# Performance work log

Hardware: AMD Instinct MI355X
Metric: run time of the kernel (lower is better)

## Reference

```python
import jax, jax.numpy as jnp
import numpy as np

EPS = 1e-5
BOUNDARY = 1.0 - EPS
TEMP = 0.5  # temperature from init_kwargs


def _safe_sqrt(t):
    # sqrt with zero (not inf/nan) gradient at t<=0; matches the analytic clamp
    # in the original custom backward (clamp(z*beta, min=eps)).
    pos = t > 0
    return jnp.where(pos, jnp.sqrt(jnp.where(pos, t, 1.0)), 0.0)


def _poincare_sim(z):
    # z: [2N, D]. Pairwise Poincare distance computed via the matmul identity
    # ||u-v||^2 = ||u||^2 + ||v||^2 - 2 u.v instead of a (2N,2N,D) broadcast.
    raw = jnp.sum(z * z, axis=-1)                      # [2N] unclamped sq norms
    sqc = jnp.clip(raw, 0.0, BOUNDARY)                 # clamped as in forward
    sqdist = jnp.maximum(raw[:, None] + raw[None, :] - 2.0 * (z @ z.T), 0.0)
    x = sqdist / ((1.0 - sqc[:, None]) * (1.0 - sqc[None, :])) * 2.0 + 1.0
    dist = jnp.log(x + _safe_sqrt(x * x - 1.0))        # arcosh(x)
    return 1.0 / (1.0 + dist)                          # Poincare similarity


def setup_inputs() -> dict:
    key = jax.random.key(0)
    k1, k2, k3, k4 = jax.random.split(key, 4)
    N, D = 4096, 8

    def ball(kg, kr):
        g = jax.random.normal(kg, (N, D), dtype=jnp.float32)
        r = jax.random.uniform(kr, (N, 1), dtype=jnp.float32) * 0.85
        return g * r / (jnp.linalg.norm(g, axis=-1, keepdims=True) + 1e-6)

    return {"z_i": ball(k1, k2), "z_j": ball(k3, k4)}


def reference(z_i, z_j):
    N = z_i.shape[0]
    z = jnp.concatenate([z_i, z_j], axis=0)            # [2N, D]
    sim = _poincare_sim(z)                             # [2N, 2N]
    idx = jnp.arange(N)
    # diag(sim, +N) and diag(sim, -N): positive pairs
    positives = jnp.concatenate([sim[idx, idx + N], sim[idx + N, idx]])  # [2N]
    mask = 1.0 - jnp.eye(2 * N, dtype=sim.dtype)       # exclude self-similarity
    denom = jnp.sum(mask * jnp.exp(sim / TEMP), axis=1)  # [2N]
    all_losses = -(positives / TEMP - jnp.log(denom))
    return jnp.sum(all_losses) / (2 * N)
```

## Files before the change

kernel.cpp:

```cpp
#include <hip/hip_runtime.h>
#include <math.h>


#define D 8
#define QS 12
#define TWO_N 8192
#define HALF_N 4096
constexpr int BLOCK = 256;
constexpr int JC    = 32;
constexpr int NTILE = 2176;
constexpr int NSEG  = 368;
constexpr int SEG_LO = 1776;
#define BOUNDARY (1.0f - 1e-5f)
#define LN2 0.6931471805599453f

typedef float f32x2 __attribute__((ext_vector_type(2)));

__device__ __forceinline__ float frcp(float x)  { return __builtin_amdgcn_rcpf(x); }
__device__ __forceinline__ float fsqrt(float x) { return __builtin_amdgcn_sqrtf(x); }
__device__ __forceinline__ float flog2(float x) { return __builtin_amdgcn_logf(x); }
__device__ __forceinline__ f32x2 splat(float v) { return (f32x2){v, v}; }

__device__ __forceinline__ float dpp_wave_sum(float v) {
    int x;
    x = __builtin_amdgcn_update_dpp(0, __float_as_int(v), 0x111, 0xf, 0xf, false);
    v += __int_as_float(x);
    x = __builtin_amdgcn_update_dpp(0, __float_as_int(v), 0x112, 0xf, 0xf, false);
    v += __int_as_float(x);
    x = __builtin_amdgcn_update_dpp(0, __float_as_int(v), 0x114, 0xf, 0xe, false);
    v += __int_as_float(x);
    x = __builtin_amdgcn_update_dpp(0, __float_as_int(v), 0x118, 0xf, 0xc, false);
    v += __int_as_float(x);
    x = __builtin_amdgcn_update_dpp(0, __float_as_int(v), 0x142, 0xa, 0xf, false);
    v += __int_as_float(x);
    x = __builtin_amdgcn_update_dpp(0, __float_as_int(v), 0x143, 0xc, 0xf, false);
    v += __int_as_float(x);
    return v;
}

__global__ __launch_bounds__(256) void prep_kernel(
    const float* __restrict__ zi, const float* __restrict__ zj,
    float* __restrict__ q, float* __restrict__ denom, float* __restrict__ out,
    float2* __restrict__ tab)
{
    const int row = blockIdx.x * 256 + threadIdx.x;
    const float* src = (row < HALF_N) ? (zi + (size_t)row * D)
                                      : (zj + (size_t)(row - HALF_N) * D);
    float4 a = *(const float4*)(src);
    float4 b = *(const float4*)(src + 4);
    float raw = a.x*a.x + a.y*a.y + a.z*a.z + a.w*a.w
              + b.x*b.x + b.y*b.y + b.z*b.z + b.w*b.w;
    float inv = frcp(1.0f - fminf(raw, BOUNDARY));
    float* dst = q + (size_t)row * QS;
    *(float4*)(dst)     = a;
    *(float4*)(dst + 4) = b;
    *(float4*)(dst + 8) = make_float4(inv, inv * raw, 0.0f, 0.0f);
    denom[row] = 0.0f;
    if (row == 0) out[0] = 0.0f;

    if (row < NSEG) {
        const int m0 = row + SEG_LO;
        const int m1 = m0 + 1;
        float ua_f = __uint_as_float(((unsigned)(m0 >> 4) << 23) | ((unsigned)(m0 & 15) << 19));
        float ub_f = __uint_as_float(((unsigned)(m1 >> 4) << 23) | ((unsigned)(m1 & 15) << 19));
        double ua = (double)ua_f, ub = (double)ub_f;
        double ga = exp(2.0 / (1.0 + log(1.0 + ua + sqrt(ua * (ua + 2.0)))));
        double gb = exp(2.0 / (1.0 + log(1.0 + ub + sqrt(ub * (ub + 2.0)))));
        double sl = (gb - ga) / (ub - ua);
        double ic = ga - sl * ua;
        tab[row] = make_float2((float)sl, (float)ic);
    }
}

struct QCol { float4 a; float4 b; float2 c; };

__device__ __forceinline__ f32x2 dot_col(const f32x2* __restrict__ p2,
                                         const QCol& qc)
{
    f32x2 x = splat(0.0f);
    x = __builtin_elementwise_fma(p2[0], splat(qc.a.x), x);
    x = __builtin_elementwise_fma(p2[1], splat(qc.a.y), x);
    x = __builtin_elementwise_fma(p2[2], splat(qc.a.z), x);
    x = __builtin_elementwise_fma(p2[3], splat(qc.a.w), x);
    x = __builtin_elementwise_fma(p2[4], splat(qc.b.x), x);
    x = __builtin_elementwise_fma(p2[5], splat(qc.b.y), x);
    x = __builtin_elementwise_fma(p2[6], splat(qc.b.z), x);
    x = __builtin_elementwise_fma(p2[7], splat(qc.b.w), x);
    x = __builtin_elementwise_fma(p2[8], splat(qc.c.x), x);
    x = __builtin_elementwise_fma(p2[9], splat(qc.c.y), x);
    return x;
}

__device__ __forceinline__ float lut1(float u, const float2* __restrict__ tab)
{
    int t = (int)(__float_as_uint(u) >> 19) - SEG_LO;
    t = (t < 0) ? 0 : t;
    t = (t > NSEG - 1) ? NSEG - 1 : t;
    float2 si = tab[t];
    return fmaf(si.x, u, si.y);
}

__global__ __launch_bounds__(BLOCK, 4) void pair_kernel(
    const float* __restrict__ q, const float2* __restrict__ gtab,
    float* __restrict__ denom)
{
    __shared__ alignas(16) float2 stab[NSEG];
    __shared__ float swave[4][JC];

    const int tid = threadIdx.x;

    const int t = blockIdx.x;
    int b = 0;
    #pragma unroll
    for (int k = 1; k < 16; ++k)
        b += (t >= (256 * k - 8 * k * (k - 1))) ? 1 : 0;
    const int Fb    = 256 * b - 8 * b * (b - 1);
    const int ibase = 512 * b;
    const int jbase = ibase + 32 * (t - Fb);
    const bool diag = (jbase < ibase + 512);

    if (tid < NSEG / 2)
        ((float4*)stab)[tid] = ((const float4*)gtab)[tid];

    const int irow0 = ibase + tid;
    const int irow1 = ibase + tid + BLOCK;
    f32x2 p2[10];
    {
        const float* q0 = q + (size_t)irow0 * QS;
        const float* q1 = q + (size_t)irow1 * QS;
        float4 a0 = *(const float4*)(q0), b0 = *(const float4*)(q0 + 4);
        float4 c0 = *(const float4*)(q0 + 8);
        float4 a1 = *(const float4*)(q1), b1 = *(const float4*)(q1 + 4);
        float4 c1 = *(const float4*)(q1 + 8);
        float m0 = -4.0f * c0.x, m1 = -4.0f * c1.x;
        p2[0] = (f32x2){m0 * a0.x, m1 * a1.x};
        p2[1] = (f32x2){m0 * a0.y, m1 * a1.y};
        p2[2] = (f32x2){m0 * a0.z, m1 * a1.z};
        p2[3] = (f32x2){m0 * a0.w, m1 * a1.w};
        p2[4] = (f32x2){m0 * b0.x, m1 * b1.x};
        p2[5] = (f32x2){m0 * b0.y, m1 * b1.y};
        p2[6] = (f32x2){m0 * b0.z, m1 * b1.z};
        p2[7] = (f32x2){m0 * b0.w, m1 * b1.w};
        p2[8] = (f32x2){2.0f * c0.y, 2.0f * c1.y};
        p2[9] = (f32x2){2.0f * c0.x, 2.0f * c1.x};
    }
    f32x2 acc2 = splat(0.0f);
    float colacc[JC];
    #pragma unroll
    for (int c = 0; c < JC; ++c) colacc[c] = 0.0f;

    __syncthreads();

    #pragma unroll
    for (int g = 0; g < JC / 4; ++g) {
        QCol qg[4];
        #pragma unroll
        for (int c = 0; c < 4; ++c) {
            const float* qc = q + (size_t)(jbase + g * 4 + c) * QS;
            qg[c].a = *(const float4*)(qc);
            qg[c].b = *(const float4*)(qc + 4);
            qg[c].c = *(const float2*)(qc + 8);
        }
        #pragma unroll
        for (int cp = 0; cp < 2; ++cp) {
            const int jj0 = g * 4 + 2 * cp, jj1 = jj0 + 1;

            f32x2 u0 = dot_col(p2, qg[2 * cp]);
            f32x2 u1 = dot_col(p2, qg[2 * cp + 1]);
            u0 = __builtin_elementwise_max(u0, splat(0.0f));
            u1 = __builtin_elementwise_max(u1, splat(0.0f));
            f32x2 e0 = (f32x2){lut1(u0.x, stab), lut1(u0.y, stab)};
            f32x2 e1 = (f32x2){lut1(u1.x, stab), lut1(u1.y, stab)};

            if (diag) {
                const int j0 = jbase + jj0, j1 = jbase + jj1;
                e0.x = (j0 > irow0) ? e0.x : 0.0f;
                e0.y = (j0 > irow1) ? e0.y : 0.0f;
                e1.x = (j1 > irow0) ? e1.x : 0.0f;
                e1.y = (j1 > irow1) ? e1.y : 0.0f;
            }
            acc2 += e0;
            acc2 += e1;
            colacc[jj0] += e0.x + e0.y;
            colacc[jj1] += e1.x + e1.y;
        }
    }

    const int wid  = tid >> 6;
    const bool l63 = ((tid & 63) == 63);
    #pragma unroll
    for (int c = 0; c < JC; ++c) {
        float s = dpp_wave_sum(colacc[c]);
        if (l63) swave[wid][c] = s;
    }

    __syncthreads();
    if (tid < JC) {
        float tot = swave[0][tid] + swave[1][tid] + swave[2][tid] + swave[3][tid];
        atomicAdd(&denom[jbase + tid], tot);
    }
    atomicAdd(&denom[irow0], acc2.x);
    atomicAdd(&denom[irow1], acc2.y);
}

__global__ __launch_bounds__(1024) void reduce_kernel(
    const float* __restrict__ zi, const float* __restrict__ zj,
    const float* __restrict__ denom, float* __restrict__ out)
{
    __shared__ float s_red[1024];
    const int tid = threadIdx.x;
    const int i   = blockIdx.x * 1024 + tid;

    const int base = (i < HALF_N) ? i : (i - HALF_N);
    const float* pa = (i < HALF_N) ? (zi + (size_t)base * D) : (zj + (size_t)base * D);
    const float* pb = (i < HALF_N) ? (zj + (size_t)base * D) : (zi + (size_t)base * D);
    float4 a0 = *(const float4*)(pa), a1 = *(const float4*)(pa + 4);
    float4 b0 = *(const float4*)(pb), b1 = *(const float4*)(pb + 4);
    float rawa = a0.x*a0.x + a0.y*a0.y + a0.z*a0.z + a0.w*a0.w
               + a1.x*a1.x + a1.y*a1.y + a1.z*a1.z + a1.w*a1.w;
    float rawb = b0.x*b0.x + b0.y*b0.y + b0.z*b0.z + b0.w*b0.w
               + b1.x*b1.x + b1.y*b1.y + b1.z*b1.z + b1.w*b1.w;
    float dot  = a0.x*b0.x + a0.y*b0.y + a0.z*b0.z + a0.w*b0.w
               + a1.x*b1.x + a1.y*b1.y + a1.z*b1.z + a1.w*b1.w;
    float sqd  = fmaxf(rawa + rawb - 2.0f * dot, 0.0f);
    float inva = frcp(1.0f - fminf(rawa, BOUNDARY));
    float invb = frcp(1.0f - fminf(rawb, BOUNDARY));
    float x    = fmaf(2.0f * sqd, inva * invb, 1.0f);
    float t    = fmaf(x, x, -1.0f);
    float s    = fsqrt(fmaxf(t, 0.0f));
    float dist = flog2(x + s) * LN2;
    float sim  = frcp(1.0f + dist);
    float dlog = flog2(denom[i]) * LN2;
    float term = -(2.0f * sim - dlog);

    s_red[tid] = term;
    __syncthreads();
    for (int off = 512; off > 0; off >>= 1) {
        if (tid < off) s_red[tid] += s_red[tid + off];
        __syncthreads();
    }
    if (tid == 0) atomicAdd(out, s_red[0] * (1.0f / (float)TWO_N));
}

extern "C" void kernel_launch(void* const* d_in, const int* in_sizes, int n_in,
                              void* d_out, int out_size, void* d_ws, size_t ws_size,
                              hipStream_t stream) {
    const float* zi = (const float*)d_in[0];
    const float* zj = (const float*)d_in[1];

    float*  denom = (float*)d_ws;
    float*  q     = denom + TWO_N;
    float2* tab   = (float2*)(q + (size_t)TWO_N * QS);

    prep_kernel<<<TWO_N / 256, 256, 0, stream>>>(zi, zj, q, denom, (float*)d_out, tab);

    pair_kernel<<<NTILE, BLOCK, 0, stream>>>(q, tab, denom);

    reduce_kernel<<<TWO_N / 1024, 1024, 0, stream>>>(zi, zj, denom, (float*)d_out);
}
```

Before: 87.31 us.

## Enlarge pair-kernel row tile to four rows per thread and DPP reduce

```diff
diff --git a/kernel.cpp b/kernel.cpp
--- a/kernel.cpp
+++ b/kernel.cpp
@@ -8,7 +8,8 @@
 #define HALF_N 4096
 constexpr int BLOCK = 256;
 constexpr int JC    = 32;
-constexpr int NTILE = 2176;
+constexpr int ITILE = 1024;
+constexpr int NTILE = 1152;
 constexpr int NSEG  = 368;
 constexpr int SEG_LO = 1776;
 #define BOUNDARY (1.0f - 1e-5f)
@@ -100,7 +101,29 @@
     return fmaf(si.x, u, si.y);
 }
 
-__global__ __launch_bounds__(BLOCK, 4) void pair_kernel(
+__device__ __forceinline__ void build_p2(const float* __restrict__ q,
+                                         int r0, int r1, f32x2* p2)
+{
+    const float* q0 = q + (size_t)r0 * QS;
+    const float* q1 = q + (size_t)r1 * QS;
+    float4 a0 = *(const float4*)(q0), b0 = *(const float4*)(q0 + 4);
+    float4 c0 = *(const float4*)(q0 + 8);
+    float4 a1 = *(const float4*)(q1), b1 = *(const float4*)(q1 + 4);
+    float4 c1 = *(const float4*)(q1 + 8);
+    float m0 = -4.0f * c0.x, m1 = -4.0f * c1.x;
+    p2[0] = (f32x2){m0 * a0.x, m1 * a1.x};
+    p2[1] = (f32x2){m0 * a0.y, m1 * a1.y};
+    p2[2] = (f32x2){m0 * a0.z, m1 * a1.z};
+    p2[3] = (f32x2){m0 * a0.w, m1 * a1.w};
+    p2[4] = (f32x2){m0 * b0.x, m1 * b1.x};
+    p2[5] = (f32x2){m0 * b0.y, m1 * b1.y};
+    p2[6] = (f32x2){m0 * b0.z, m1 * b1.z};
+    p2[7] = (f32x2){m0 * b0.w, m1 * b1.w};
+    p2[8] = (f32x2){2.0f * c0.y, 2.0f * c1.y};
+    p2[9] = (f32x2){2.0f * c0.x, 2.0f * c1.x};
+}
+
+__global__ __launch_bounds__(BLOCK) void pair_kernel(
     const float* __restrict__ q, const float2* __restrict__ gtab,
     float* __restrict__ denom)
 {
@@ -112,39 +135,25 @@
     const int t = blockIdx.x;
     int b = 0;
     #pragma unroll
-    for (int k = 1; k < 16; ++k)
-        b += (t >= (256 * k - 8 * k * (k - 1))) ? 1 : 0;
-    const int Fb    = 256 * b - 8 * b * (b - 1);
-    const int ibase = 512 * b;
+    for (int k = 1; k < 8; ++k)
+        b += (t >= (256 * k - 16 * k * (k - 1))) ? 1 : 0;
+    const int Fb    = 256 * b - 16 * b * (b - 1);
+    const int ibase = ITILE * b;
     const int jbase = ibase + 32 * (t - Fb);
-    const bool diag = (jbase < ibase + 512);
+    const bool diag = (jbase < ibase + ITILE);
 
     if (tid < NSEG / 2)
         ((float4*)stab)[tid] = ((const float4*)gtab)[tid];
 
     const int irow0 = ibase + tid;
-    const int irow1 = ibase + tid + BLOCK;
-    f32x2 p2[10];
-    {
-        const float* q0 = q + (size_t)irow0 * QS;
-        const float* q1 = q + (size_t)irow1 * QS;
-        float4 a0 = *(const float4*)(q0), b0 = *(const float4*)(q0 + 4);
-        float4 c0 = *(const float4*)(q0 + 8);
-        float4 a1 = *(const float4*)(q1), b1 = *(const float4*)(q1 + 4);
-        float4 c1 = *(const float4*)(q1 + 8);
-        float m0 = -4.0f * c0.x, m1 = -4.0f * c1.x;
-        p2[0] = (f32x2){m0 * a0.x, m1 * a1.x};
-        p2[1] = (f32x2){m0 * a0.y, m1 * a1.y};
-        p2[2] = (f32x2){m0 * a0.z, m1 * a1.z};
-        p2[3] = (f32x2){m0 * a0.w, m1 * a1.w};
-        p2[4] = (f32x2){m0 * b0.x, m1 * b1.x};
-        p2[5] = (f32x2){m0 * b0.y, m1 * b1.y};
-        p2[6] = (f32x2){m0 * b0.z, m1 * b1.z};
-        p2[7] = (f32x2){m0 * b0.w, m1 * b1.w};
-        p2[8] = (f32x2){2.0f * c0.y, 2.0f * c1.y};
-        p2[9] = (f32x2){2.0f * c0.x, 2.0f * c1.x};
-    }
-    f32x2 acc2 = splat(0.0f);
+    const int irow1 = irow0 + 256;
+    const int irow2 = irow0 + 512;
+    const int irow3 = irow0 + 768;
+    f32x2 pA[10], pB[10];
+    build_p2(q, irow0, irow1, pA);
+    build_p2(q, irow2, irow3, pB);
+
+    f32x2 accA = splat(0.0f), accB = splat(0.0f);
     float colacc[JC];
     #pragma unroll
     for (int c = 0; c < JC; ++c) colacc[c] = 0.0f;
@@ -152,38 +161,46 @@
     __syncthreads();
 
     #pragma unroll
-    for (int g = 0; g < JC / 4; ++g) {
-        QCol qg[4];
-        #pragma unroll
-        for (int c = 0; c < 4; ++c) {
-            const float* qc = q + (size_t)(jbase + g * 4 + c) * QS;
-            qg[c].a = *(const float4*)(qc);
-            qg[c].b = *(const float4*)(qc + 4);
-            qg[c].c = *(const float2*)(qc + 8);
+    for (int jp = 0; jp < JC / 2; ++jp) {
+        const int jj0 = 2 * jp, jj1 = 2 * jp + 1;
+        const float* qc0 = q + (size_t)(jbase + jj0) * QS;
+
+        QCol q0, q1;
+        q0.a = *(const float4*)(qc0);
+        q0.b = *(const float4*)(qc0 + 4);
+        q0.c = *(const float2*)(qc0 + 8);
+        q1.a = *(const float4*)(qc0 + QS);
+        q1.b = *(const float4*)(qc0 + QS + 4);
+        q1.c = *(const float2*)(qc0 + QS + 8);
+
+        f32x2 uA0 = dot_col(pA, q0);
+        f32x2 uB0 = dot_col(pB, q0);
+        f32x2 uA1 = dot_col(pA, q1);
+        f32x2 uB1 = dot_col(pB, q1);
+        uA0 = __builtin_elementwise_max(uA0, splat(0.0f));
+        uB0 = __builtin_elementwise_max(uB0, splat(0.0f));
+        uA1 = __builtin_elementwise_max(uA1, splat(0.0f));
+        uB1 = __builtin_elementwise_max(uB1, splat(0.0f));
+        f32x2 eA0 = (f32x2){lut1(uA0.x, stab), lut1(uA0.y, stab)};
+        f32x2 eB0 = (f32x2){lut1(uB0.x, stab), lut1(uB0.y, stab)};
+        f32x2 eA1 = (f32x2){lut1(uA1.x, stab), lut1(uA1.y, stab)};
+        f32x2 eB1 = (f32x2){lut1(uB1.x, stab), lut1(uB1.y, stab)};
+
+        if (diag) {
+            const int j0 = jbase + jj0, j1 = jbase + jj1;
+            eA0.x = (j0 > irow0) ? eA0.x : 0.0f;
+            eA0.y = (j0 > irow1) ? eA0.y : 0.0f;
+            eB0.x = (j0 > irow2) ? eB0.x : 0.0f;
+            eB0.y = (j0 > irow3) ? eB0.y : 0.0f;
+            eA1.x = (j1 > irow0) ? eA1.x : 0.0f;
+            eA1.y = (j1 > irow1) ? eA1.y : 0.0f;
+            eB1.x = (j1 > irow2) ? eB1.x : 0.0f;
+            eB1.y = (j1 > irow3) ? eB1.y : 0.0f;
         }
-        #pragma unroll
-        for (int cp = 0; cp < 2; ++cp) {
-            const int jj0 = g * 4 + 2 * cp, jj1 = jj0 + 1;
-
-            f32x2 u0 = dot_col(p2, qg[2 * cp]);
-            f32x2 u1 = dot_col(p2, qg[2 * cp + 1]);
-            u0 = __builtin_elementwise_max(u0, splat(0.0f));
-            u1 = __builtin_elementwise_max(u1, splat(0.0f));
-            f32x2 e0 = (f32x2){lut1(u0.x, stab), lut1(u0.y, stab)};
-            f32x2 e1 = (f32x2){lut1(u1.x, stab), lut1(u1.y, stab)};
-
-            if (diag) {
-                const int j0 = jbase + jj0, j1 = jbase + jj1;
-                e0.x = (j0 > irow0) ? e0.x : 0.0f;
-                e0.y = (j0 > irow1) ? e0.y : 0.0f;
-                e1.x = (j1 > irow0) ? e1.x : 0.0f;
-                e1.y = (j1 > irow1) ? e1.y : 0.0f;
-            }
-            acc2 += e0;
-            acc2 += e1;
-            colacc[jj0] += e0.x + e0.y;
-            colacc[jj1] += e1.x + e1.y;
-        }
+        accA += eA0; accA += eA1;
+        accB += eB0; accB += eB1;
+        colacc[jj0] += (eA0.x + eA0.y) + (eB0.x + eB0.y);
+        colacc[jj1] += (eA1.x + eA1.y) + (eB1.x + eB1.y);
     }
 
     const int wid  = tid >> 6;
@@ -199,17 +216,19 @@
         float tot = swave[0][tid] + swave[1][tid] + swave[2][tid] + swave[3][tid];
         atomicAdd(&denom[jbase + tid], tot);
     }
-    atomicAdd(&denom[irow0], acc2.x);
-    atomicAdd(&denom[irow1], acc2.y);
-}
-
-__global__ __launch_bounds__(1024) void reduce_kernel(
+    atomicAdd(&denom[irow0], accA.x);
+    atomicAdd(&denom[irow1], accA.y);
+    atomicAdd(&denom[irow2], accB.x);
+    atomicAdd(&denom[irow3], accB.y);
+}
+
+__global__ __launch_bounds__(256) void reduce_kernel(
     const float* __restrict__ zi, const float* __restrict__ zj,
     const float* __restrict__ denom, float* __restrict__ out)
 {
-    __shared__ float s_red[1024];
+    __shared__ float swred[4];
     const int tid = threadIdx.x;
-    const int i   = blockIdx.x * 1024 + tid;
+    const int i   = blockIdx.x * 256 + tid;
 
     const int base = (i < HALF_N) ? i : (i - HALF_N);
     const float* pa = (i < HALF_N) ? (zi + (size_t)base * D) : (zj + (size_t)base * D);
@@ -233,13 +252,12 @@
     float dlog = flog2(denom[i]) * LN2;
     float term = -(2.0f * sim - dlog);
 
-    s_red[tid] = term;
+    float ws = dpp_wave_sum(term);
+    if ((tid & 63) == 63) swred[tid >> 6] = ws;
     __syncthreads();
-    for (int off = 512; off > 0; off >>= 1) {
-        if (tid < off) s_red[tid] += s_red[tid + off];
-        __syncthreads();
-    }
-    if (tid == 0) atomicAdd(out, s_red[0] * (1.0f / (float)TWO_N));
+    if (tid == 0)
+        atomicAdd(out, (swred[0] + swred[1] + swred[2] + swred[3])
+                           * (1.0f / (float)TWO_N));
 }
 
 extern "C" void kernel_launch(void* const* d_in, const int* in_sizes, int n_in,
@@ -256,5 +274,5 @@
 
     pair_kernel<<<NTILE, BLOCK, 0, stream>>>(q, tab, denom);
 
-    reduce_kernel<<<TWO_N / 1024, 1024, 0, stream>>>(zi, zj, denom, (float*)d_out);
-}
+    reduce_kernel<<<TWO_N / 256, 256, 0, stream>>>(zi, zj, denom, (float*)d_out);
+}
```

After: 92.08 us. 5.5% more time.
